# Kernel tuning notes

Measured on AMD Instinct MI355X. Metric: run time of the kernel, lower is better.

The kernel has to match this reference:

```python
import jax, jax.numpy as jnp
import numpy as np

B, N, D, H = 2, 2048, 768, 12
HD = D // H


def setup_inputs() -> dict:
    key = jax.random.key(0)
    ks = jax.random.split(key, 8)
    x = jax.random.normal(ks[0], (B, N, D), dtype=jnp.float32)
    dist = jax.random.randint(ks[1], (B, N, N), 0, 32, dtype=jnp.int32)
    mask = jax.random.bernoulli(ks[2], 0.1, (B, N))  # True = masked key
    # parameters (torch Linear stored pre-transposed: y = x @ W + b)
    s = 1.0 / np.sqrt(D)
    qkv_w = jax.random.uniform(ks[3], (D, 3 * D), jnp.float32, -s, s)
    qkv_b = jax.random.uniform(ks[4], (3 * D,), jnp.float32, -s, s)
    out_w = jax.random.uniform(ks[5], (D, D), jnp.float32, -s, s)
    out_b = jax.random.uniform(ks[6], (D,), jnp.float32, -s, s)
    bias_table = jax.random.normal(ks[7], (32, H), dtype=jnp.float32)
    return {"x": x, "dist": dist, "mask": mask, "qkv_w": qkv_w,
            "qkv_b": qkv_b, "out_w": out_w, "out_b": out_b,
            "bias_table": bias_table}


def reference(x, dist, mask, qkv_w, qkv_b, out_w, out_b, bias_table):
    scale = HD ** -0.5
    qkv = x @ qkv_w + qkv_b                      # [B,N,3D]
    q, k, v = jnp.split(qkv, 3, axis=-1)
    sh = lambda t: t.reshape(B, N, H, HD).transpose(0, 2, 1, 3)  # [B,H,N,HD]
    q, k, v = sh(q), sh(k), sh(v)
    a = jnp.einsum('bhnd,bhmd->bhnm', q, k) * scale  # [B,H,N,N]
    # relative-position bias: gather [B,N,N,H] -> [B,H,N,N]
    a = a + bias_table[jnp.clip(dist, 0, 31)].transpose(0, 3, 1, 2)
    a = jnp.where(mask[:, None, None, :], -jnp.inf, a)
    a = jax.nn.softmax(a.astype(jnp.float32), axis=-1)  # dropout: eval mode (p ignored)
    o = jnp.einsum('bhnm,bhmd->bhnd', a, v)            # [B,H,N,HD]
    o = o.transpose(0, 2, 1, 3).reshape(B, N, D)
    return o @ out_w + out_b
```

## Files before the change

kernel.cpp:

```cpp
#include <hip/hip_runtime.h>
#include <hip/hip_bf16.h>

typedef unsigned short u16;
typedef __attribute__((ext_vector_type(8))) short bf16x8;
typedef __attribute__((ext_vector_type(4))) short bf16x4;
typedef __attribute__((ext_vector_type(4))) float f32x4;

#define MFMA_BF16(a,b,c) __builtin_amdgcn_mfma_f32_16x16x32_bf16((a),(b),(c),0,0,0)
#define LOG2E 1.4426950408889634f

#if __has_builtin(__builtin_amdgcn_mfma_f32_16x16x16bf16_1k)
#define MFMA16(a,b,c) __builtin_amdgcn_mfma_f32_16x16x16bf16_1k((a),(b),(c),0,0,0)
#define HAVE_MFMA16 1
#elif __has_builtin(__builtin_amdgcn_mfma_f32_16x16x16_bf16)
#define MFMA16(a,b,c) __builtin_amdgcn_mfma_f32_16x16x16_bf16((a),(b),(c),0,0,0)
#define HAVE_MFMA16 1
#else
#define HAVE_MFMA16 0
#endif

__device__ __forceinline__ u16 f2b(float f) {
    __hip_bfloat16 h = __float2bfloat16(f);
    u16 u; __builtin_memcpy(&u, &h, 2); return u;
}
__device__ __forceinline__ f32x4 zero4() { f32x4 z = {0.f,0.f,0.f,0.f}; return z; }

__device__ __forceinline__ void gl_lds16(const u16* g, u16* l) {
    __builtin_amdgcn_global_load_lds(
        (const __attribute__((address_space(1))) unsigned int*)g,
        (__attribute__((address_space(3))) unsigned int*)l,
        16, 0, 0);
}

__global__ __launch_bounds__(256)
void prep(const float* __restrict__ x, u16* __restrict__ xb,
          const float* __restrict__ qkv_w, u16* __restrict__ wqkvT,
          const float* __restrict__ out_w, u16* __restrict__ woutT,
          const int* __restrict__ dist, const unsigned* __restrict__ mask,
          unsigned char* __restrict__ dist8) {
    __shared__ __align__(16) u16 T[64][68];
    __shared__ int sB, sH, sF;
    const int bid = blockIdx.x;
    const int tid = threadIdx.x;
    if (bid < 8192) {
        if (tid == 0) { sB = 0; sH = 0; sF = 0; }
        __syncthreads();
        int lb = 0, lh = 0, lf = 0;
#pragma unroll
        for (int i = 0; i < 4; ++i) {
            unsigned v = mask[tid + i * 256];
            if (v == 0x3f800000u) { lf = 1; }
            else if (v > 1u) {
                unsigned b0 = v & 0xffu, b1 = (v >> 8) & 0xffu, b2 = (v >> 16) & 0xffu, b3 = v >> 24;
                bool bytesOK = (b0 <= 1u) && (b1 <= 1u) && (b2 <= 1u) && (b3 <= 1u);
                unsigned h0 = v & 0xffffu, h1 = v >> 16;
                bool halfOK = (h0 == 0u || h0 == 0x3f80u) && (h1 == 0u || h1 == 0x3f80u);
                if (bytesOK) lb = 1; else if (halfOK) lh = 1;
            }
        }
        if (lb) atomicOr(&sB, 1);
        if (lh) atomicOr(&sH, 1);
        if (lf) atomicOr(&sF, 1);
        __syncthreads();
        int mode = sH ? 3 : (sB ? 1 : (sF ? 2 : 0));
        size_t i = ((size_t)bid * 256 + tid) * 4;
        int4 v = *(const int4*)(dist + i);
        int b = (int)(i >> 22), j = (int)(i & 2047);
        int base = b * 2048 + j;
        int mk0, mk1, mk2, mk3;
        if (mode == 0) {
            int4 mv = *(const int4*)((const int*)mask + base);
            mk0 = mv.x != 0; mk1 = mv.y != 0; mk2 = mv.z != 0; mk3 = mv.w != 0;
        } else if (mode == 1) {
            const unsigned char* m8 = (const unsigned char*)mask;
            mk0 = m8[base] != 0; mk1 = m8[base+1] != 0; mk2 = m8[base+2] != 0; mk3 = m8[base+3] != 0;
        } else if (mode == 2) {
            float4 mv = *(const float4*)((const float*)mask + base);
            mk0 = mv.x != 0.f; mk1 = mv.y != 0.f; mk2 = mv.z != 0.f; mk3 = mv.w != 0.f;
        } else {
            const u16* mh = (const u16*)mask;
            mk0 = mh[base] != 0; mk1 = mh[base+1] != 0; mk2 = mh[base+2] != 0; mk3 = mh[base+3] != 0;
        }
        uchar4 o;
        o.x = mk0 ? 32 : (unsigned char)min(max(v.x, 0), 31);
        o.y = mk1 ? 32 : (unsigned char)min(max(v.y, 0), 31);
        o.z = mk2 ? 32 : (unsigned char)min(max(v.z, 0), 31);
        o.w = mk3 ? 32 : (unsigned char)min(max(v.w, 0), 31);
        *(uchar4*)(dist8 + i) = o;
    } else if (bid < 8192 + 1536) {
        size_t i = ((size_t)(bid - 8192) * 256 + tid) * 8;
        float4 a = *(const float4*)(x + i);
        float4 b = *(const float4*)(x + i + 4);
        union { u16 s[8]; uint4 v; } u;
        u.s[0]=f2b(a.x); u.s[1]=f2b(a.y); u.s[2]=f2b(a.z); u.s[3]=f2b(a.w);
        u.s[4]=f2b(b.x); u.s[5]=f2b(b.y); u.s[6]=f2b(b.z); u.s[7]=f2b(b.w);
        *(uint4*)(xb + i) = u.v;
    } else {
        const float* in; u16* out; int C, c0, k0;
        if (bid < 8192 + 1536 + 432) {
            int s = bid - (8192 + 1536);
            in = qkv_w; out = wqkvT; C = 2304;
            c0 = (s % 36) * 64; k0 = (s / 36) * 64;
        } else {
            int s = bid - (8192 + 1536 + 432);
            in = out_w; out = woutT; C = 768;
            c0 = (s % 12) * 64; k0 = (s / 12) * 64;
        }
#pragma unroll
        for (int i = 0; i < 4; ++i) {
            int id = tid + i * 256;
            int row = id >> 4, ch = id & 15;
            float4 v = *(const float4*)(in + (size_t)(k0 + row) * C + c0 + ch * 4);
            T[row][ch*4+0] = f2b(v.x); T[row][ch*4+1] = f2b(v.y);
            T[row][ch*4+2] = f2b(v.z); T[row][ch*4+3] = f2b(v.w);
        }
        __syncthreads();
#pragma unroll
        for (int i = 0; i < 2; ++i) {
            int id = tid + i * 256;
            int c = id >> 3, ch = id & 7;
            union { u16 s[8]; uint4 v; } u;
#pragma unroll
            for (int jj = 0; jj < 8; ++jj) u.s[jj] = T[ch*8+jj][c];
            *(uint4*)(out + (size_t)(c0 + c) * 768 + k0 + ch * 8) = u.v;
        }
    }
}

template<int MODE>
__global__ __launch_bounds__(256)
void gemmBT(const u16* __restrict__ A, const u16* __restrict__ Bt,
            const float* __restrict__ bias,
            u16* __restrict__ qO, u16* __restrict__ kO, u16* __restrict__ vO,
            float* __restrict__ fO) {
    __shared__ __align__(16) u16 As[2][128*32];
    __shared__ __align__(16) u16 Bs[2][128*32];
    const int K = 768;
    const int tid = threadIdx.x;
    const int lane = tid & 63, w = tid >> 6;
    const int wm = w >> 1, wn = w & 1;
    const int l15 = lane & 15, q = lane >> 4;
    const int m0 = blockIdx.y * 128, n0 = blockIdx.x * 128;
    const int stRow = (lane >> 2);
    const int stChunk = (lane & 3) ^ ((lane >> 3) & 3);
    const u16* Ag = A + (size_t)(m0 + w*32 + stRow) * K + stChunk * 8;
    const u16* Bg = Bt + (size_t)(n0 + w*32 + stRow) * K + stChunk * 8;
    u16* ldsA = &As[0][0] + w*32*32;
    u16* ldsB = &Bs[0][0] + w*32*32;
    const int fA = (q ^ ((l15 >> 1) & 3)) * 8;

    f32x4 acc[4][4];
#pragma unroll
    for (int i=0;i<4;++i)
#pragma unroll
        for (int j=0;j<4;++j) acc[i][j] = zero4();

#pragma unroll
    for (int c = 0; c < 2; ++c) {
        gl_lds16(Ag + (size_t)(c*16) * K, ldsA + c*16*32);
        gl_lds16(Bg + (size_t)(c*16) * K, ldsB + c*16*32);
    }
    __syncthreads();

    int cur = 0;
    for (int kt = 0; kt < 24; ++kt) {
        if (kt < 23) {
            const int ko = (kt + 1) * 32;
            u16* dA = &As[cur^1][0] + w*32*32;
            u16* dB = &Bs[cur^1][0] + w*32*32;
#pragma unroll
            for (int c = 0; c < 2; ++c) {
                gl_lds16(Ag + (size_t)(c*16) * K + ko, dA + c*16*32);
                gl_lds16(Bg + (size_t)(c*16) * K + ko, dB + c*16*32);
            }
        }
        const u16* as = &As[cur][0];
        const u16* bs = &Bs[cur][0];
        bf16x8 af[4], bfr[4];
#pragma unroll
        for (int mt=0; mt<4; ++mt) af[mt]  = *(const bf16x8*)(as + (wm*64+mt*16+l15)*32 + fA);
#pragma unroll
        for (int nt=0; nt<4; ++nt) bfr[nt] = *(const bf16x8*)(bs + (wn*64+nt*16+l15)*32 + fA);
#pragma unroll
        for (int mt=0; mt<4; ++mt)
#pragma unroll
            for (int nt=0; nt<4; ++nt)
                acc[mt][nt] = MFMA_BF16(af[mt], bfr[nt], acc[mt][nt]);
        __syncthreads();
        cur ^= 1;
    }

#pragma unroll
    for (int mt=0; mt<4; ++mt) {
#pragma unroll
        for (int nt=0; nt<4; ++nt) {
            int n = n0 + wn*64 + nt*16 + l15;
            float bv = bias[n];
            if (MODE == 0) {
                int which = n / 768;
                int rem = n - which*768;
                int hh = rem >> 6, hd = rem & 63;
                int mBase = m0 + wm*64 + mt*16 + q*4;
                int b = mBase >> 11, tok0 = mBase & 2047;
                if (which == 2) {
                    union { u16 s4[4]; unsigned long long u; } pv;
#pragma unroll
                    for (int r=0; r<4; ++r) pv.s4[r] = f2b(acc[mt][nt][r] + bv);
                    *(unsigned long long*)(vO + ((size_t)(b*12 + hh)*64 + hd)*2048 + tok0) = pv.u;
                } else {
#pragma unroll
                    for (int r=0; r<4; ++r) {
                        float v = acc[mt][nt][r] + bv;
                        size_t di = (((size_t)(b*12 + hh))*2048 + tok0 + r)*64 + hd;
                        if (which == 0) qO[di] = f2b(v * (0.125f * LOG2E));
                        else            kO[di] = f2b(v);
                    }
                }
            } else {
#pragma unroll
                for (int r=0; r<4; ++r) {
                    int m = m0 + wm*64 + mt*16 + q*4 + r;
                    fO[(size_t)m*768 + n] = acc[mt][nt][r] + bv;
                }
            }
        }
    }
}

__global__ __launch_bounds__(256)
void gemmOut(const u16* __restrict__ A, const u16* __restrict__ Bt,
             const float* __restrict__ bias, float* __restrict__ fO) {
    __shared__ __align__(16) u16 As[2][64*32];
    __shared__ __align__(16) u16 Bs[2][64*32];
    const int K = 768;
    const int tid = threadIdx.x;
    const int lane = tid & 63, w = tid >> 6;
    const int l15 = lane & 15, q = lane >> 4;
    const int m0 = blockIdx.y * 64, n0 = blockIdx.x * 64;
    const int stRow = tid >> 2;
    const int stChunk = (tid & 3) ^ ((tid >> 3) & 3);
    const u16* Ag = A + (size_t)(m0 + stRow) * K + stChunk * 8;
    const u16* Bg = Bt + (size_t)(n0 + stRow) * K + stChunk * 8;
    const int fA = (q ^ ((l15 >> 1) & 3)) * 8;

    f32x4 acc[4];
#pragma unroll
    for (int i=0;i<4;++i) acc[i] = zero4();

    gl_lds16(Ag, &As[0][0] + w*512);
    gl_lds16(Bg, &Bs[0][0] + w*512);
    __syncthreads();

    int cur = 0;
    for (int kt = 0; kt < 24; ++kt) {
        if (kt < 23) {
            const int ko = (kt + 1) * 32;
            gl_lds16(Ag + ko, &As[cur^1][0] + w*512);
            gl_lds16(Bg + ko, &Bs[cur^1][0] + w*512);
        }
        const u16* as = &As[cur][0];
        const u16* bs = &Bs[cur][0];
        bf16x8 af = *(const bf16x8*)(as + (w*16 + l15)*32 + fA);
        bf16x8 bfr[4];
#pragma unroll
        for (int nt=0; nt<4; ++nt) bfr[nt] = *(const bf16x8*)(bs + (nt*16+l15)*32 + fA);
#pragma unroll
        for (int nt=0; nt<4; ++nt) acc[nt] = MFMA_BF16(af, bfr[nt], acc[nt]);
        __syncthreads();
        cur ^= 1;
    }

#pragma unroll
    for (int nt=0; nt<4; ++nt) {
        int n = n0 + nt*16 + l15;
        float bv = bias[n];
#pragma unroll
        for (int r=0; r<4; ++r) {
            int m = m0 + w*16 + q*4 + r;
            fO[(size_t)m*768 + n] = acc[nt][r] + bv;
        }
    }
}

__global__ __launch_bounds__(256)
void flashAttn(const u16* __restrict__ Qb, const u16* __restrict__ Kb,
               const u16* __restrict__ Vt, const unsigned char* __restrict__ dist8,
               const float* __restrict__ btg, u16* __restrict__ attnout) {
    __shared__ float bt[33];
    __shared__ __align__(16) u16 KT[2][4096];
    __shared__ __align__(16) u16 VT[2][4096];
    __shared__ __align__(16) u16 DT[2][2048];
    __shared__ __align__(16) u16 Os[4][16][72];
    const int tid = threadIdx.x;
    const int lane = tid & 63, w = tid >> 6;
    const int l15 = lane & 15, q = lane >> 4;
    const int wg = blockIdx.x + 32 * (blockIdx.y + 12 * blockIdx.z);
    const int xcd = wg & 7, slot = wg >> 3;
    const int g = ((slot >> 5) << 3) + xcd;
    const int i0 = (slot & 31) * 64;
    const int b = g / 12, h = g - b * 12;
    const int bh = g;
    const float NEG_INF = -__builtin_inff();
    if (tid < 33) bt[tid] = (tid == 32) ? NEG_INF : btg[tid*12 + h] * LOG2E;

    const int iRow = i0 + w*16 + l15;
    const u16* Qp = Qb + ((size_t)bh*2048 + iRow)*64;
    bf16x8 qB0 = *(const bf16x8*)(Qp + q*8);
    bf16x8 qB1 = *(const bf16x8*)(Qp + 32 + q*8);
#if !HAVE_MFMA16
    const int srcL0 = ((2*q)   & 3)*16 + l15;
    const int srcL1 = ((2*q+1) & 3)*16 + l15;
    union { unsigned u4[4]; bf16x8 v; } one_;
    { unsigned oc = (l15 == 0) ? 0x3F803F80u : 0u;
      one_.u4[0]=oc; one_.u4[1]=oc; one_.u4[2]=oc; one_.u4[3]=oc; }
#else
    union { unsigned u2[2]; bf16x4 v; } one4_;
    { unsigned oc = (l15 == 0) ? 0x3F803F80u : 0u;
      one4_.u2[0]=oc; one4_.u2[1]=oc; }
#endif

    const int stRow = w*16 + (lane >> 3);
    const int stCol = (((lane & 7) ^ (lane >> 3)) << 4);
    const int dRow = w*16 + (lane >> 2);
    const int dCol = ((lane & 3) ^ ((lane >> 3) & 3)) << 4;
    const char* kgB = (const char*)Kb + (size_t)bh*2048*128;
    const char* vgB = (const char*)Vt + (size_t)bh*64*4096;
    const unsigned char* dgB = dist8 + (size_t)(b*2048 + i0)*2048;
    const int swz = (l15 & 7) << 4;
    const int f0 = (q*16)      ^ swz;
    const int f1 = (q*16 + 64) ^ swz;
    const int rB = l15 * 128;
    const int rD = (w*16 + l15) * 64;
    const int dsw = (l15 >> 1) & 3;

    {
        u16* kd = &KT[0][0] + w*1024;
        u16* vd = &VT[0][0] + w*1024;
#pragma unroll
        for (int c = 0; c < 2; ++c) {
            int row = stRow + c*8;
            gl_lds16((const u16*)(kgB + (size_t)row*128 + stCol),  kd + c*512);
            gl_lds16((const u16*)(vgB + (size_t)row*4096 + stCol), vd + c*512);
        }
        gl_lds16((const u16*)(dgB + (size_t)dRow*2048 + dCol),
                 (u16*)((char*)&DT[0][0] + w*1024));
    }
    __syncthreads();

    f32x4 o0 = zero4(), o1 = zero4(), o2 = zero4(), o3 = zero4(), o4 = zero4();
    float mI = NEG_INF;
    int cur = 0;

    for (int jt = 0; jt < 32; ++jt) {
        const int j0 = jt * 64;
        if (jt < 31) {
            const int j0n = j0 + 64;
            u16* kd = &KT[cur^1][0] + w*1024;
            u16* vd = &VT[cur^1][0] + w*1024;
#pragma unroll
            for (int c = 0; c < 2; ++c) {
                int row = stRow + c*8;
                gl_lds16((const u16*)(kgB + (size_t)(j0n + row)*128 + stCol),          kd + c*512);
                gl_lds16((const u16*)(vgB + (size_t)row*4096 + (size_t)j0n*2 + stCol), vd + c*512);
            }
            gl_lds16((const u16*)(dgB + (size_t)dRow*2048 + j0n + dCol),
                     (u16*)((char*)&DT[cur^1][0] + w*1024));
        }
        const char* dt = (const char*)&DT[cur][0];
        unsigned dv4[4];
#pragma unroll
        for (int mt = 0; mt < 4; ++mt)
            dv4[mt] = *(const unsigned*)(dt + rD + ((mt ^ dsw) << 4) + q*4);

        const char* kt = (const char*)&KT[cur][0];
        f32x4 s0 = zero4(), s1 = zero4(), s2 = zero4(), s3 = zero4();
        {
            bf16x8 k00 = *(const bf16x8*)(kt + rB          + f0);
            bf16x8 k01 = *(const bf16x8*)(kt + rB          + f1);
            bf16x8 k10 = *(const bf16x8*)(kt + rB + 2048   + f0);
            bf16x8 k11 = *(const bf16x8*)(kt + rB + 2048   + f1);
            bf16x8 k20 = *(const bf16x8*)(kt + rB + 4096   + f0);
            bf16x8 k21 = *(const bf16x8*)(kt + rB + 4096   + f1);
            bf16x8 k30 = *(const bf16x8*)(kt + rB + 6144   + f0);
            bf16x8 k31 = *(const bf16x8*)(kt + rB + 6144   + f1);
            __builtin_amdgcn_s_setprio(1);
            s0 = MFMA_BF16(k00, qB0, s0); s0 = MFMA_BF16(k01, qB1, s0);
            s1 = MFMA_BF16(k10, qB0, s1); s1 = MFMA_BF16(k11, qB1, s1);
            s2 = MFMA_BF16(k20, qB0, s2); s2 = MFMA_BF16(k21, qB1, s2);
            s3 = MFMA_BF16(k30, qB0, s3); s3 = MFMA_BF16(k31, qB1, s3);
            __builtin_amdgcn_s_setprio(0);
        }

        float sv[4][4];
#pragma unroll
        for (int mt = 0; mt < 4; ++mt) {
            const f32x4 sm = mt==0 ? s0 : (mt==1 ? s1 : (mt==2 ? s2 : s3));
            const unsigned d4 = dv4[mt];
#pragma unroll
            for (int r = 0; r < 4; ++r) {
                int dd = (d4 >> (r*8)) & 255;
                sv[mt][r] = sm[r] + bt[dd];
            }
        }

        float t0 = fmaxf(fmaxf(sv[0][0], sv[0][1]), fmaxf(sv[0][2], sv[0][3]));
        float t1 = fmaxf(fmaxf(sv[1][0], sv[1][1]), fmaxf(sv[1][2], sv[1][3]));
        float t2 = fmaxf(fmaxf(sv[2][0], sv[2][1]), fmaxf(sv[2][2], sv[2][3]));
        float t3 = fmaxf(fmaxf(sv[3][0], sv[3][1]), fmaxf(sv[3][2], sv[3][3]));
        float rm = fmaxf(fmaxf(t0, t1), fmaxf(t2, t3));
        rm = fmaxf(rm, __shfl_xor(rm, 16, 64));
        rm = fmaxf(rm, __shfl_xor(rm, 32, 64));
        if (!__all(rm <= mI)) {
            float mn = fmaxf(mI, rm);
            float al = exp2f(mI - mn);
            mI = mn;
#pragma unroll
            for (int r = 0; r < 4; ++r) { o0[r] *= al; o1[r] *= al; o2[r] *= al; o3[r] *= al; }
            o4[0] *= al;
        }
        float p[4][4];
#pragma unroll
        for (int mt = 0; mt < 4; ++mt)
#pragma unroll
            for (int r = 0; r < 4; ++r) p[mt][r] = exp2f(sv[mt][r] - mI);

        const char* vt = (const char*)&VT[cur][0];
#if HAVE_MFMA16
        __builtin_amdgcn_s_setprio(1);
#pragma unroll
        for (int mt = 0; mt < 4; ++mt) {
            union { unsigned d[2]; bf16x4 v; } pu;
            pu.d[0] = (unsigned)f2b(p[mt][0]) | ((unsigned)f2b(p[mt][1]) << 16);
            pu.d[1] = (unsigned)f2b(p[mt][2]) | ((unsigned)f2b(p[mt][3]) << 16);
            const int cbase = (((mt*2 + (q>>1)) ^ (l15 & 7)) << 4) + (q & 1)*8;
            bf16x4 v0 = *(const bf16x4*)(vt + rB          + cbase);
            bf16x4 v1 = *(const bf16x4*)(vt + rB + 2048   + cbase);
            bf16x4 v2 = *(const bf16x4*)(vt + rB + 4096   + cbase);
            bf16x4 v3 = *(const bf16x4*)(vt + rB + 6144   + cbase);
            o0 = MFMA16(v0, pu.v, o0);
            o1 = MFMA16(v1, pu.v, o1);
            o2 = MFMA16(v2, pu.v, o2);
            o3 = MFMA16(v3, pu.v, o3);
            o4 = MFMA16(one4_.v, pu.v, o4);
        }
        __builtin_amdgcn_s_setprio(0);
#else
        unsigned pk[4][2];
#pragma unroll
        for (int mt = 0; mt < 4; ++mt) {
            pk[mt][0] = (unsigned)f2b(p[mt][0]) | ((unsigned)f2b(p[mt][1]) << 16);
            pk[mt][1] = (unsigned)f2b(p[mt][2]) | ((unsigned)f2b(p[mt][3]) << 16);
        }
        __builtin_amdgcn_s_setprio(1);
#pragma unroll
        for (int ks = 0; ks < 2; ++ks) {
            union { unsigned d[4]; bf16x8 v; } pb;
#pragma unroll
            for (int s = 0; s < 4; ++s) {
                int sl = (s >> 1) ? srcL1 : srcL0;
                int u0 = __shfl((int)pk[2*ks    ][s & 1], sl, 64);
                int u1 = __shfl((int)pk[2*ks + 1][s & 1], sl, 64);
                pb.d[s] = (q >> 1) ? (unsigned)u1 : (unsigned)u0;
            }
            const int fk = ks ? f1 : f0;
            bf16x8 v0 = *(const bf16x8*)(vt + rB          + fk);
            bf16x8 v1 = *(const bf16x8*)(vt + rB + 2048   + fk);
            bf16x8 v2 = *(const bf16x8*)(vt + rB + 4096   + fk);
            bf16x8 v3 = *(const bf16x8*)(vt + rB + 6144   + fk);
            o0 = MFMA_BF16(v0, pb.v, o0);
            o1 = MFMA_BF16(v1, pb.v, o1);
            o2 = MFMA_BF16(v2, pb.v, o2);
            o3 = MFMA_BF16(v3, pb.v, o3);
            o4 = MFMA_BF16(one_.v, pb.v, o4);
        }
        __builtin_amdgcn_s_setprio(0);
#endif

        __syncthreads();
        cur ^= 1;
    }

    float lsum = __shfl(o4[0], l15, 64);
    float inv = 1.0f / lsum;
#pragma unroll
    for (int r = 0; r < 4; ++r) {
        Os[w][l15][ 0 + q*4 + r] = f2b(o0[r] * inv);
        Os[w][l15][16 + q*4 + r] = f2b(o1[r] * inv);
        Os[w][l15][32 + q*4 + r] = f2b(o2[r] * inv);
        Os[w][l15][48 + q*4 + r] = f2b(o3[r] * inv);
    }
    __syncthreads();
    int rr = lane >> 2, cc = lane & 3;
    uint4 a0 = *(const uint4*)&Os[w][rr][cc*16];
    uint4 a1 = *(const uint4*)&Os[w][rr][cc*16 + 8];
    size_t orow = ((size_t)b*2048 + i0 + w*16 + rr)*768 + h*64 + cc*16;
    *(uint4*)(attnout + orow)     = a0;
    *(uint4*)(attnout + orow + 8) = a1;
}

extern "C" void kernel_launch(void* const* d_in, const int* in_sizes, int n_in,
                              void* d_out, int out_size, void* d_ws, size_t ws_size,
                              hipStream_t stream) {
    (void)in_sizes; (void)n_in; (void)out_size; (void)ws_size;
    const float* x      = (const float*)d_in[0];
    const int*   dist   = (const int*)d_in[1];
    const int*   mask   = (const int*)d_in[2];
    const float* qkv_w  = (const float*)d_in[3];
    const float* qkv_b  = (const float*)d_in[4];
    const float* out_w  = (const float*)d_in[5];
    const float* out_b  = (const float*)d_in[6];
    const float* btab   = (const float*)d_in[7];
    float* out = (float*)d_out;

    char* ws = (char*)d_ws;
    size_t off = 0;
    auto alloc = [&](size_t bytes) { void* p = ws + off; off += (bytes + 255) & ~(size_t)255; return p; };
    u16* xb      = (u16*)alloc((size_t)4096*768*2);
    u16* wqkvT   = (u16*)alloc((size_t)2304*768*2);
    u16* woutT   = (u16*)alloc((size_t)768*768*2);
    u16* Qb      = (u16*)alloc((size_t)24*2048*64*2);
    u16* Kb      = (u16*)alloc((size_t)24*2048*64*2);
    u16* Vtp     = (u16*)alloc((size_t)24*2048*64*2);
    u16* attnout = (u16*)alloc((size_t)4096*768*2);
    unsigned char* dist8 = (unsigned char*)alloc((size_t)2*2048*2048);

    prep<<<8192 + 1536 + 432 + 144, 256, 0, stream>>>(
        x, xb, qkv_w, wqkvT, out_w, woutT, dist, (const unsigned*)mask, dist8);
    gemmBT<0><<<dim3(18,32), 256, 0, stream>>>(xb, wqkvT, qkv_b, Qb, Kb, Vtp, nullptr);
    flashAttn<<<dim3(32,12,2), 256, 0, stream>>>(Qb, Kb, Vtp, dist8, btab, attnout);
    gemmOut<<<dim3(12,64), 256, 0, stream>>>(attnout, woutT, out_b, out);
}
```

Measured before the change: 227.6 us.

## Shrink QKV GEMM tile, stage Q/K epilogue through LDS, relax softmax rescale

The QKV projection GEMM now uses 64x128 tiles, doubling the grid from 576 to 1152 blocks so more CUs stay busy. Its Q/K epilogue is staged in shared memory, so each head row is written with coalesced 16-byte stores instead of scattered 2-byte stores. Separately, the flash-attention online softmax now skips the rescale of running outputs unless the row max rises by more than 8 in log2 units. That lazy rescale saves exp and multiply work per tile, but it lets exponents grow up to 2^8 before rescaling, a small overflow or precision risk in fp32.

```diff
diff --git a/kernel.cpp b/kernel.cpp
--- a/kernel.cpp
+++ b/kernel.cpp
@@ -127,102 +127,102 @@
     }
 }
 
-template<int MODE>
 __global__ __launch_bounds__(256)
-void gemmBT(const u16* __restrict__ A, const u16* __restrict__ Bt,
-            const float* __restrict__ bias,
-            u16* __restrict__ qO, u16* __restrict__ kO, u16* __restrict__ vO,
-            float* __restrict__ fO) {
-    __shared__ __align__(16) u16 As[2][128*32];
+void gemmQKV(const u16* __restrict__ A, const u16* __restrict__ Bt,
+             const float* __restrict__ bias,
+             u16* __restrict__ qO, u16* __restrict__ kO, u16* __restrict__ vO) {
+    __shared__ __align__(16) u16 As[2][64*32];
     __shared__ __align__(16) u16 Bs[2][128*32];
+    __shared__ __align__(16) u16 Ls[64*128];
     const int K = 768;
     const int tid = threadIdx.x;
     const int lane = tid & 63, w = tid >> 6;
-    const int wm = w >> 1, wn = w & 1;
     const int l15 = lane & 15, q = lane >> 4;
-    const int m0 = blockIdx.y * 128, n0 = blockIdx.x * 128;
-    const int stRow = (lane >> 2);
+    const int m0 = blockIdx.y * 64, n0 = blockIdx.x * 128;
+    const int stRow = lane >> 2;
     const int stChunk = (lane & 3) ^ ((lane >> 3) & 3);
-    const u16* Ag = A + (size_t)(m0 + w*32 + stRow) * K + stChunk * 8;
+    const u16* Ag = A + (size_t)(m0 + w*16 + stRow) * K + stChunk * 8;
     const u16* Bg = Bt + (size_t)(n0 + w*32 + stRow) * K + stChunk * 8;
-    u16* ldsA = &As[0][0] + w*32*32;
-    u16* ldsB = &Bs[0][0] + w*32*32;
     const int fA = (q ^ ((l15 >> 1) & 3)) * 8;
 
-    f32x4 acc[4][4];
+    f32x4 acc[4][2];
 #pragma unroll
     for (int i=0;i<4;++i)
 #pragma unroll
-        for (int j=0;j<4;++j) acc[i][j] = zero4();
-
-#pragma unroll
-    for (int c = 0; c < 2; ++c) {
-        gl_lds16(Ag + (size_t)(c*16) * K, ldsA + c*16*32);
-        gl_lds16(Bg + (size_t)(c*16) * K, ldsB + c*16*32);
-    }
+        for (int j=0;j<2;++j) acc[i][j] = zero4();
+
+    gl_lds16(Ag, &As[0][0] + w*16*32);
+#pragma unroll
+    for (int c = 0; c < 2; ++c)
+        gl_lds16(Bg + (size_t)(c*16) * K, &Bs[0][0] + (w*32 + c*16)*32);
     __syncthreads();
 
     int cur = 0;
     for (int kt = 0; kt < 24; ++kt) {
         if (kt < 23) {
             const int ko = (kt + 1) * 32;
-            u16* dA = &As[cur^1][0] + w*32*32;
-            u16* dB = &Bs[cur^1][0] + w*32*32;
-#pragma unroll
-            for (int c = 0; c < 2; ++c) {
-                gl_lds16(Ag + (size_t)(c*16) * K + ko, dA + c*16*32);
-                gl_lds16(Bg + (size_t)(c*16) * K + ko, dB + c*16*32);
-            }
+            gl_lds16(Ag + ko, &As[cur^1][0] + w*16*32);
+#pragma unroll
+            for (int c = 0; c < 2; ++c)
+                gl_lds16(Bg + (size_t)(c*16) * K + ko, &Bs[cur^1][0] + (w*32 + c*16)*32);
         }
         const u16* as = &As[cur][0];
         const u16* bs = &Bs[cur][0];
-        bf16x8 af[4], bfr[4];
-#pragma unroll
-        for (int mt=0; mt<4; ++mt) af[mt]  = *(const bf16x8*)(as + (wm*64+mt*16+l15)*32 + fA);
-#pragma unroll
-        for (int nt=0; nt<4; ++nt) bfr[nt] = *(const bf16x8*)(bs + (wn*64+nt*16+l15)*32 + fA);
+        bf16x8 af[4], bfr[2];
+#pragma unroll
+        for (int mt=0; mt<4; ++mt) af[mt]  = *(const bf16x8*)(as + (mt*16+l15)*32 + fA);
+#pragma unroll
+        for (int nt=0; nt<2; ++nt) bfr[nt] = *(const bf16x8*)(bs + (w*32+nt*16+l15)*32 + fA);
 #pragma unroll
         for (int mt=0; mt<4; ++mt)
 #pragma unroll
-            for (int nt=0; nt<4; ++nt)
+            for (int nt=0; nt<2; ++nt)
                 acc[mt][nt] = MFMA_BF16(af[mt], bfr[nt], acc[mt][nt]);
         __syncthreads();
         cur ^= 1;
     }
 
-#pragma unroll
-    for (int mt=0; mt<4; ++mt) {
-#pragma unroll
-        for (int nt=0; nt<4; ++nt) {
-            int n = n0 + wn*64 + nt*16 + l15;
-            float bv = bias[n];
-            if (MODE == 0) {
-                int which = n / 768;
-                int rem = n - which*768;
+    const int which = n0 / 768;
+    const int b = m0 >> 11, tokB = m0 & 2047;
+    if (which == 2) {
+#pragma unroll
+        for (int mt=0; mt<4; ++mt) {
+#pragma unroll
+            for (int nt=0; nt<2; ++nt) {
+                int n = n0 + w*32 + nt*16 + l15;
+                int rem = n - 1536;
                 int hh = rem >> 6, hd = rem & 63;
-                int mBase = m0 + wm*64 + mt*16 + q*4;
-                int b = mBase >> 11, tok0 = mBase & 2047;
-                if (which == 2) {
-                    union { u16 s4[4]; unsigned long long u; } pv;
-#pragma unroll
-                    for (int r=0; r<4; ++r) pv.s4[r] = f2b(acc[mt][nt][r] + bv);
-                    *(unsigned long long*)(vO + ((size_t)(b*12 + hh)*64 + hd)*2048 + tok0) = pv.u;
-                } else {
-#pragma unroll
-                    for (int r=0; r<4; ++r) {
-                        float v = acc[mt][nt][r] + bv;
-                        size_t di = (((size_t)(b*12 + hh))*2048 + tok0 + r)*64 + hd;
-                        if (which == 0) qO[di] = f2b(v * (0.125f * LOG2E));
-                        else            kO[di] = f2b(v);
-                    }
-                }
-            } else {
-#pragma unroll
-                for (int r=0; r<4; ++r) {
-                    int m = m0 + wm*64 + mt*16 + q*4 + r;
-                    fO[(size_t)m*768 + n] = acc[mt][nt][r] + bv;
-                }
+                float bv = bias[n];
+                int tok0 = tokB + mt*16 + q*4;
+                union { u16 s4[4]; unsigned long long u; } pv;
+#pragma unroll
+                for (int r=0; r<4; ++r) pv.s4[r] = f2b(acc[mt][nt][r] + bv);
+                *(unsigned long long*)(vO + ((size_t)(b*12 + hh)*64 + hd)*2048 + tok0) = pv.u;
             }
+        }
+    } else {
+        const float sc = (which == 0) ? (0.125f * LOG2E) : 1.0f;
+#pragma unroll
+        for (int mt=0; mt<4; ++mt) {
+#pragma unroll
+            for (int nt=0; nt<2; ++nt) {
+                int nl = w*32 + nt*16 + l15;
+                float bv = bias[n0 + nl];
+#pragma unroll
+                for (int r=0; r<4; ++r)
+                    Ls[(mt*16 + q*4 + r)*128 + nl] = f2b((acc[mt][nt][r] + bv) * sc);
+            }
+        }
+        __syncthreads();
+        u16* dst = (which == 0) ? qO : kO;
+        const int h0 = (n0 - which*768) >> 6;
+#pragma unroll
+        for (int k = 0; k < 4; ++k) {
+            int idx = k*256 + tid;
+            int row = idx >> 4, rem = idx & 15;
+            int hh = rem >> 3, c = rem & 7;
+            uint4 v = *(const uint4*)(Ls + row*128 + hh*64 + c*8);
+            *(uint4*)(dst + ((size_t)(b*12 + h0 + hh)*2048 + tokB + row)*64 + c*8) = v;
         }
     }
 }
@@ -410,7 +410,7 @@
         float rm = fmaxf(fmaxf(t0, t1), fmaxf(t2, t3));
         rm = fmaxf(rm, __shfl_xor(rm, 16, 64));
         rm = fmaxf(rm, __shfl_xor(rm, 32, 64));
-        if (!__all(rm <= mI)) {
+        if (!__all(rm <= mI + 8.0f)) {
             float mn = fmaxf(mI, rm);
             float al = exp2f(mI - mn);
             mI = mn;
@@ -526,7 +526,7 @@
 
     prep<<<8192 + 1536 + 432 + 144, 256, 0, stream>>>(
         x, xb, qkv_w, wqkvT, out_w, woutT, dist, (const unsigned*)mask, dist8);
-    gemmBT<0><<<dim3(18,32), 256, 0, stream>>>(xb, wqkvT, qkv_b, Qb, Kb, Vtp, nullptr);
+    gemmQKV<<<dim3(18,64), 256, 0, stream>>>(xb, wqkvT, qkv_b, Qb, Kb, Vtp);
     flashAttn<<<dim3(32,12,2), 256, 0, stream>>>(Qb, Kb, Vtp, dist8, btab, attnout);
     gemmOut<<<dim3(12,64), 256, 0, stream>>>(attnout, woutT, out_b, out);
 }
```

New measurement: 232.6 us. 1.02x slower.
